# Kernel optimization log

Measured on AMD Instinct MI355X. Metric: run time of the kernel, lower is better.

## Reference

```python
import jax, jax.numpy as jnp
import numpy as np

RADIUS = 3  # local window half-size -> K = (2*RADIUS+1)**2 = 49 taps


def _bilinear_sample_zeros(img_flat, x, y, h, w):
    """Bilinear sampling with zeros padding (grid_sample, align_corners=True).
    img_flat: (B, C, H*W); x, y: (P, K) pixel-space coords. Returns (B, C, P, K).
    align_corners=True denormalization exactly inverts the normalization in the
    original module, so we sample directly at pixel coordinates.
    """
    B, C, _ = img_flat.shape
    x0 = jnp.floor(x)
    y0 = jnp.floor(y)
    out = jnp.zeros((B, C) + x.shape, dtype=img_flat.dtype)
    corners = [
        (x0,       y0,       (x0 + 1 - x) * (y0 + 1 - y)),
        (x0 + 1.0, y0,       (x - x0) * (y0 + 1 - y)),
        (x0,       y0 + 1.0, (x0 + 1 - x) * (y - y0)),
        (x0 + 1.0, y0 + 1.0, (x - x0) * (y - y0)),
    ]
    for xi, yi, wt in corners:
        inb = (xi >= 0) & (xi < w) & (yi >= 0) & (yi < h)
        xi_c = jnp.clip(xi, 0, w - 1).astype(jnp.int32)
        yi_c = jnp.clip(yi, 0, h - 1).astype(jnp.int32)
        idx = (yi_c * w + xi_c).reshape(-1)            # (P*K,)
        v = jnp.take(img_flat, idx, axis=2)            # (B, C, P*K)
        v = v.reshape(B, C, *x.shape)                  # (B, C, P, K)
        out = out + v * (wt * inb.astype(img_flat.dtype))[None, None]
    return out


def reference(feature0, feature1):
    n, c, s, h, w = feature0.shape
    B = n * s
    f0 = feature0.transpose(0, 2, 1, 3, 4).reshape(B, c, h, w)
    f1 = feature1.transpose(0, 2, 1, 3, 4).reshape(B, c, h, w)

    r = RADIUS
    # base pixel coords (x, y), flattened row-major over (h, w) -> (P, 2)
    yy, xx = jnp.meshgrid(jnp.arange(h, dtype=jnp.float32),
                          jnp.arange(w, dtype=jnp.float32), indexing='ij')
    base = jnp.stack([xx, yy], axis=-1).reshape(h * w, 2)  # (P, 2)

    # window offsets (dx, dy), dy outer / dx inner ordering -> (K, 2)
    dys, dxs = jnp.meshgrid(jnp.arange(-r, r + 1, dtype=jnp.float32),
                            jnp.arange(-r, r + 1, dtype=jnp.float32), indexing='ij')
    offs = jnp.stack([dxs, dys], axis=-1).reshape(-1, 2)   # (K, 2)

    sample = base[:, None, :] + offs[None, :, :]           # (P, K, 2)
    valid = ((sample[..., 0] >= 0) & (sample[..., 0] < w) &
             (sample[..., 1] >= 0) & (sample[..., 1] < h))  # (P, K)

    f1_flat = f1.reshape(B, c, h * w)
    wf = _bilinear_sample_zeros(f1_flat, sample[..., 0], sample[..., 1], h, w)  # (B, c, P, K)

    f0_flat = f0.reshape(B, c, h * w)
    corr = jnp.einsum('bcp,bcpk->bpk', f0_flat, wf) / jnp.asarray(c, jnp.float32) ** 0.5
    corr = jnp.where(valid[None], corr, -jnp.inf)
    prob = jax.nn.softmax(corr, axis=-1)                   # (B, P, K)

    corresp = jnp.einsum('bpk,pkj->bpj', prob, sample)     # (B, P, 2) expected (x, y)
    flow = corresp - base[None]                            # (B, P, 2)
    flow = flow.reshape(n, s, h, w, 2).transpose(0, 4, 1, 2, 3)  # (n, 2, s, h, w)
    return flow


def setup_inputs() -> dict:
    key = jax.random.key(0)
    k0, k1 = jax.random.split(key)
    n, c, s, h, w = 2, 64, 4, 64, 44
    feature0 = jax.random.normal(k0, (n, c, s, h, w), dtype=jnp.float32)
    feature1 = jax.random.normal(k1, (n, c, s, h, w), dtype=jnp.float32)
    return {"feature0": feature0, "feature1": feature1}
```

## Files before the change

### kernel.cpp

```cpp
#include <hip/hip_runtime.h>
#include <math.h>

#define N_  2
#define C_  64
#define S_  4
#define H_  64
#define W_  44
#define HW_       (H_ * W_)
#define CH_STRIDE (S_ * HW_)
#define NSTRIDE   (C_ * S_ * HW_)

typedef _Float16 h8 __attribute__((ext_vector_type(8)));
typedef float    f4 __attribute__((ext_vector_type(4)));

__global__ __launch_bounds__(512) void repack_kernel(
    const float* __restrict__ f0,
    const float* __restrict__ f1,
    _Float16* __restrict__ pk0,
    _Float16* __restrict__ pk1)
{
    const int tid = threadIdx.x;
    const int c8  = tid >> 6;
    const int xi  = tid & 63;
    const int b   = blockIdx.x & 7;
    const int y   = blockIdx.x >> 3;
    const int n_idx = b >> 2;
    const int s_idx = b & 3;
    const int base  = n_idx * NSTRIDE + s_idx * HW_ + y * W_;

    {
        const int col  = xi - 8;
        const bool vld = (col >= 0) && (col < W_);
        const int cc   = min(max(col, 0), W_ - 1);
        const float* p = f1 + base + cc;
        float v[8];
        #pragma unroll
        for (int j = 0; j < 8; ++j)
            v[j] = p[(size_t)(c8 * 8 + j) * CH_STRIDE];
        h8 pk;
        #pragma unroll
        for (int j = 0; j < 8; ++j)
            pk[j] = vld ? (_Float16)v[j] : (_Float16)0.0f;
        *(h8*)&pk1[(((size_t)(b * 64 + y) * 8 + c8) << 9) + xi * 8] = pk;
    }

    if (xi < 48) {
        const bool vld = (xi < W_);
        const int xc   = min(xi, W_ - 1);
        const float* p = f0 + base + xc;
        float v[8];
        #pragma unroll
        for (int j = 0; j < 8; ++j)
            v[j] = p[(size_t)(c8 * 8 + j) * CH_STRIDE];
        h8 pk;
        #pragma unroll
        for (int j = 0; j < 8; ++j)
            pk[j] = vld ? (_Float16)v[j] : (_Float16)0.0f;
        *(h8*)&pk0[(size_t)(b * 64 + y) * 3072 + (c8 * 48 + xi) * 8] = pk;
    }
}

__global__ __launch_bounds__(448) void flow_main(
    const _Float16* __restrict__ pk0,
    const _Float16* __restrict__ pk1,
    float* __restrict__ out)
{
    const int lane = threadIdx.x & 63;
    const int w    = threadIdx.x >> 6;
    const int b    = blockIdx.x & 7;
    const int y    = blockIdx.x >> 3;
    const int n_idx = b >> 2;
    const int s_idx = b & 3;

    __shared__ float corr[W_][49];

    const int row = y + w - 3;
    if (row >= 0 && row < H_) {
        const int quad = lane >> 4;
        const int l16  = lane & 15;

        const h8* A = (const h8*)(pk0 + (size_t)(b * 64 + y) * 3072);
        const h8* B = (const h8*)(pk1 + ((size_t)(b * 64 + row) << 12));

        h8 afr[3][2], bfr[3][2][2];
        #pragma unroll
        for (int mi = 0; mi < 3; ++mi) {
            #pragma unroll
            for (int kh = 0; kh < 2; ++kh) {
                afr[mi][kh] = A[(kh * 4 + quad) * 48 + mi * 16 + l16];
                #pragma unroll
                for (int nh = 0; nh < 2; ++nh)
                    bfr[mi][nh][kh] =
                        B[(kh * 4 + quad) * 64 + mi * 16 + nh * 16 + l16];
            }
        }

        f4 acc[3][2];
        #pragma unroll
        for (int mi = 0; mi < 3; ++mi) {
            #pragma unroll
            for (int nh = 0; nh < 2; ++nh) {
                f4 a = {0.f, 0.f, 0.f, 0.f};
                #pragma unroll
                for (int kh = 0; kh < 2; ++kh)
                    a = __builtin_amdgcn_mfma_f32_16x16x32_f16(
                            afr[mi][kh], bfr[mi][nh][kh], a, 0, 0, 0);
                acc[mi][nh] = a;
            }
        }

        #pragma unroll
        for (int mi = 0; mi < 3; ++mi) {
            #pragma unroll
            for (int nh = 0; nh < 2; ++nh) {
                #pragma unroll
                for (int r = 0; r < 4; ++r) {
                    const int x   = mi * 16 + quad * 4 + r;
                    const int col = mi * 16 + nh * 16 - 8 + l16;
                    const int dx  = col - x + 3;
                    if (x < W_ && dx >= 0 && dx < 7)
                        corr[x][w * 7 + dx] = acc[mi][nh][r] * 0.125f;
                }
            }
        }
    }

    __syncthreads();

    if (w == 0) {
        const int xe = min(lane, W_ - 1);
        float c[49];
        float m = -1e30f;
        #pragma unroll
        for (int k = 0; k < 49; ++k) {
            const int kdy = k / 7, kdx = k % 7;
            const int col = lane + kdx - 3;
            const int rr  = y + kdy - 3;
            const bool ok = (col >= 0) && (col < W_) && (rr >= 0) && (rr < H_);
            const float v = ok ? corr[xe][k] : -1e30f;
            c[k] = v;
            m = fmaxf(m, v);
        }
        float S = 0.0f, Sx = 0.0f, Sy = 0.0f;
        #pragma unroll
        for (int k = 0; k < 49; ++k) {
            const float e = __expf(c[k] - m);
            S  += e;
            Sx += e * (float)(k % 7 - 3);
            Sy += e * (float)(k / 7 - 3);
        }
        if (lane < W_) {
            const float inv = 1.0f / S;
            const int ob = (n_idx * 2) * S_ * HW_ + s_idx * HW_ + y * W_ + lane;
            out[ob]            = Sx * inv;
            out[ob + S_ * HW_] = Sy * inv;
        }
    }
}

extern "C" void kernel_launch(void* const* d_in, const int* in_sizes, int n_in,
                              void* d_out, int out_size, void* d_ws, size_t ws_size,
                              hipStream_t stream) {
    const float* f0 = (const float*)d_in[0];
    const float* f1 = (const float*)d_in[1];
    float* out = (float*)d_out;

    _Float16* pk1 = (_Float16*)d_ws;
    _Float16* pk0 = pk1 + (size_t)8 * 64 * 8 * 512;

    repack_kernel<<<8 * H_, 512, 0, stream>>>(f0, f1, pk0, pk1);
    flow_main<<<8 * H_, 448, 0, stream>>>(pk0, pk1, out);
}
```

Baseline: 68.14 us.

## Fuse fp16 repack into main flow kernel, loading fp32 inputs directly

Drops the separate repack kernel that converted inputs to a packed fp16 workspace layout. The main kernel now reads fp32 features straight from the original strided layout and converts them to fp16 in registers before the MFMAs. This removes one kernel launch and the workspace write and read round trip. In exchange it issues strided scalar loads with a channel stride, and each row of f1 is re-read by up to seven blocks and converted again.

```diff
diff --git a/kernel.cpp b/kernel.cpp
--- a/kernel.cpp
+++ b/kernel.cpp
@@ -13,56 +13,9 @@
 typedef _Float16 h8 __attribute__((ext_vector_type(8)));
 typedef float    f4 __attribute__((ext_vector_type(4)));
 
-__global__ __launch_bounds__(512) void repack_kernel(
+__global__ __launch_bounds__(448) void flow_kernel(
     const float* __restrict__ f0,
     const float* __restrict__ f1,
-    _Float16* __restrict__ pk0,
-    _Float16* __restrict__ pk1)
-{
-    const int tid = threadIdx.x;
-    const int c8  = tid >> 6;
-    const int xi  = tid & 63;
-    const int b   = blockIdx.x & 7;
-    const int y   = blockIdx.x >> 3;
-    const int n_idx = b >> 2;
-    const int s_idx = b & 3;
-    const int base  = n_idx * NSTRIDE + s_idx * HW_ + y * W_;
-
-    {
-        const int col  = xi - 8;
-        const bool vld = (col >= 0) && (col < W_);
-        const int cc   = min(max(col, 0), W_ - 1);
-        const float* p = f1 + base + cc;
-        float v[8];
-        #pragma unroll
-        for (int j = 0; j < 8; ++j)
-            v[j] = p[(size_t)(c8 * 8 + j) * CH_STRIDE];
-        h8 pk;
-        #pragma unroll
-        for (int j = 0; j < 8; ++j)
-            pk[j] = vld ? (_Float16)v[j] : (_Float16)0.0f;
-        *(h8*)&pk1[(((size_t)(b * 64 + y) * 8 + c8) << 9) + xi * 8] = pk;
-    }
-
-    if (xi < 48) {
-        const bool vld = (xi < W_);
-        const int xc   = min(xi, W_ - 1);
-        const float* p = f0 + base + xc;
-        float v[8];
-        #pragma unroll
-        for (int j = 0; j < 8; ++j)
-            v[j] = p[(size_t)(c8 * 8 + j) * CH_STRIDE];
-        h8 pk;
-        #pragma unroll
-        for (int j = 0; j < 8; ++j)
-            pk[j] = vld ? (_Float16)v[j] : (_Float16)0.0f;
-        *(h8*)&pk0[(size_t)(b * 64 + y) * 3072 + (c8 * 48 + xi) * 8] = pk;
-    }
-}
-
-__global__ __launch_bounds__(448) void flow_main(
-    const _Float16* __restrict__ pk0,
-    const _Float16* __restrict__ pk1,
     float* __restrict__ out)
 {
     const int lane = threadIdx.x & 63;
@@ -71,6 +24,7 @@
     const int y    = blockIdx.x >> 3;
     const int n_idx = b >> 2;
     const int s_idx = b & 3;
+    const int base  = n_idx * NSTRIDE + s_idx * HW_;
 
     __shared__ float corr[W_][49];
 
@@ -79,32 +33,51 @@
         const int quad = lane >> 4;
         const int l16  = lane & 15;
 
-        const h8* A = (const h8*)(pk0 + (size_t)(b * 64 + y) * 3072);
-        const h8* B = (const h8*)(pk1 + ((size_t)(b * 64 + row) << 12));
-
-        h8 afr[3][2], bfr[3][2][2];
+        h8 afr[3][2];
         #pragma unroll
         for (int mi = 0; mi < 3; ++mi) {
+            const int  x  = mi * 16 + l16;
+            const bool av = (x < W_);
+            const float* pa = f0 + base + y * W_ + (av ? x : 0);
             #pragma unroll
             for (int kh = 0; kh < 2; ++kh) {
-                afr[mi][kh] = A[(kh * 4 + quad) * 48 + mi * 16 + l16];
+                const int ch0 = (kh * 4 + quad) * 8;
+                float v[8];
                 #pragma unroll
-                for (int nh = 0; nh < 2; ++nh)
-                    bfr[mi][nh][kh] =
-                        B[(kh * 4 + quad) * 64 + mi * 16 + nh * 16 + l16];
+                for (int j = 0; j < 8; ++j)
+                    v[j] = pa[(size_t)(ch0 + j) * CH_STRIDE];
+                h8 a;
+                #pragma unroll
+                for (int j = 0; j < 8; ++j)
+                    a[j] = av ? (_Float16)v[j] : (_Float16)0.0f;
+                afr[mi][kh] = a;
             }
         }
 
+        const float* pb_row = f1 + base + row * W_;
         f4 acc[3][2];
         #pragma unroll
         for (int mi = 0; mi < 3; ++mi) {
             #pragma unroll
             for (int nh = 0; nh < 2; ++nh) {
+                const int  col = mi * 16 + nh * 16 - 8 + l16;
+                const bool bv  = (col >= 0) && (col < W_);
+                const float* pb = pb_row + (bv ? col : 0);
                 f4 a = {0.f, 0.f, 0.f, 0.f};
                 #pragma unroll
-                for (int kh = 0; kh < 2; ++kh)
+                for (int kh = 0; kh < 2; ++kh) {
+                    const int ch0 = (kh * 4 + quad) * 8;
+                    float v[8];
+                    #pragma unroll
+                    for (int j = 0; j < 8; ++j)
+                        v[j] = pb[(size_t)(ch0 + j) * CH_STRIDE];
+                    h8 bf;
+                    #pragma unroll
+                    for (int j = 0; j < 8; ++j)
+                        bf[j] = bv ? (_Float16)v[j] : (_Float16)0.0f;
                     a = __builtin_amdgcn_mfma_f32_16x16x32_f16(
-                            afr[mi][kh], bfr[mi][nh][kh], a, 0, 0, 0);
+                            afr[mi][kh], bf, a, 0, 0, 0);
+                }
                 acc[mi][nh] = a;
             }
         }
@@ -165,9 +138,5 @@
     const float* f1 = (const float*)d_in[1];
     float* out = (float*)d_out;
 
-    _Float16* pk1 = (_Float16*)d_ws;
-    _Float16* pk0 = pk1 + (size_t)8 * 64 * 8 * 512;
-
-    repack_kernel<<<8 * H_, 512, 0, stream>>>(f0, f1, pk0, pk1);
-    flow_main<<<8 * H_, 448, 0, stream>>>(pk0, pk1, out);
+    flow_kernel<<<8 * H_, 448, 0, stream>>>(f0, f1, out);
 }
```

Measured after the change: 68.74 us. About the same (+0.9%).
